# Kernel tuning notes

Measured on AMD Instinct MI355X. Metric: run time of the kernel, lower is better.

Reference implementation:

```python
import jax, jax.numpy as jnp
import numpy as np

N = 100000   # nodes
E = 1600000  # edges (avg degree 16)
D = 48       # in_channels
H = 256      # hidden_channels
HH = H // 2  # 128
OUT = 40     # out_channels


def _lin(key, fan_in, fan_out):
    return jax.random.normal(key, (fan_in, fan_out), jnp.float32) * (1.0 / np.sqrt(fan_in))


def setup_inputs() -> dict:
    key = jax.random.key(0)
    ks = jax.random.split(key, 8)
    node_feature = jax.random.normal(ks[0], (N, D), jnp.float32)
    edge_index = jax.random.randint(ks[1], (2, E), 0, N, dtype=jnp.int32)
    return {
        "node_feature": node_feature,
        "edge_index": edge_index,
        # mlp1: (D + D) -> H -> HH
        "W1a": _lin(ks[2], 2 * D, H), "b1a": jnp.zeros((H,), jnp.float32),
        "W1b": _lin(ks[3], H, HH),    "b1b": jnp.zeros((HH,), jnp.float32),
        # mlp2: (HH + HH + D) -> H -> HH
        "W2a": _lin(ks[4], 2 * HH + D, H), "b2a": jnp.zeros((H,), jnp.float32),
        "W2b": _lin(ks[5], H, HH),         "b2b": jnp.zeros((HH,), jnp.float32),
        # mlp3: (HH + HH + D) -> H -> OUT
        "W3a": _lin(ks[6], 2 * HH + D, H), "b3a": jnp.zeros((H,), jnp.float32),
        "W3b": _lin(ks[7], H, OUT),        "b3b": jnp.zeros((OUT,), jnp.float32),
    }


def _lgconv(x, src, dst):
    # LGConv(normalize=False): out[i] = sum_{(j,i) in E} x[j]
    return jax.ops.segment_sum(x[src], dst, num_segments=N)


def _mlp(x, Wa, ba, Wb, bb):
    # pyg MLP(-1, hidden, out): Linear -> ReLU -> Linear
    return jax.nn.relu(x @ Wa + ba) @ Wb + bb


def reference(node_feature, edge_index,
              W1a, b1a, W1b, b1b,
              W2a, b2a, W2b, b2b,
              W3a, b3a, W3b, b3b):
    src, dst = edge_index[0], edge_index[1]

    c1 = _lgconv(node_feature, src, dst)                    # [N, D]
    h1 = jax.nn.relu(_mlp(jnp.concatenate([c1, node_feature], axis=1),
                          W1a, b1a, W1b, b1b))              # [N, HH]

    c2 = _lgconv(h1, src, dst)                              # [N, HH]
    h2 = jax.nn.relu(_mlp(jnp.concatenate([c2, h1, node_feature], axis=1),
                          W2a, b2a, W2b, b2b))              # [N, HH]

    c3 = _lgconv(h2, src, dst)                              # [N, HH]
    logits = _mlp(jnp.concatenate([c3, h2, node_feature], axis=1),
                  W3a, b3a, W3b, b3b)                       # [N, OUT]
    return jax.nn.log_softmax(logits, axis=1)
```

## Files before the change

### kernel.cpp

```cpp
#include <hip/hip_runtime.h>
#include <math.h>

typedef __attribute__((ext_vector_type(8)))  short s16x8;
typedef __attribute__((ext_vector_type(16))) float f32x16;
typedef __attribute__((ext_vector_type(2)))  float f32x2;

__device__ inline unsigned short f2bf(float f) {
    unsigned u = __float_as_uint(f);
    u += 0x7fffu + ((u >> 16) & 1u);
    return (unsigned short)(u >> 16);
}
__device__ inline unsigned char f2fp8(float v) {
    return (unsigned char)(__builtin_amdgcn_cvt_pk_fp8_f32(v, v, 0, false) & 0xff);
}
__device__ inline void acc_fp8x8(float* a, uint2 v) {
    f32x2 p0 = __builtin_amdgcn_cvt_pk_f32_fp8(v.x, false);
    f32x2 p1 = __builtin_amdgcn_cvt_pk_f32_fp8(v.x, true);
    f32x2 p2 = __builtin_amdgcn_cvt_pk_f32_fp8(v.y, false);
    f32x2 p3 = __builtin_amdgcn_cvt_pk_f32_fp8(v.y, true);
    a[0] += p0.x; a[1] += p0.y; a[2] += p1.x; a[3] += p1.y;
    a[4] += p2.x; a[5] += p2.y; a[6] += p3.x; a[7] += p3.y;
}
__device__ inline uint4 fp8x8_to_bf16x8(uint2 v) {
    f32x2 p0 = __builtin_amdgcn_cvt_pk_f32_fp8(v.x, false);
    f32x2 p1 = __builtin_amdgcn_cvt_pk_f32_fp8(v.x, true);
    f32x2 p2 = __builtin_amdgcn_cvt_pk_f32_fp8(v.y, false);
    f32x2 p3 = __builtin_amdgcn_cvt_pk_f32_fp8(v.y, true);
    uint4 o;
    o.x = ((unsigned)f2bf(p0.y) << 16) | f2bf(p0.x);
    o.y = ((unsigned)f2bf(p1.y) << 16) | f2bf(p1.x);
    o.z = ((unsigned)f2bf(p2.y) << 16) | f2bf(p2.x);
    o.w = ((unsigned)f2bf(p3.y) << 16) | f2bf(p3.x);
    return o;
}

#define BMAX 3200
#define RNG  512

__global__ __launch_bounds__(256)
void prep_fused(const float* __restrict__ x,
                unsigned char* __restrict__ xq,
                const float* __restrict__ W1a, unsigned short* __restrict__ Wf1a,
                const float* __restrict__ W1b, unsigned short* __restrict__ Wf1b,
                const float* __restrict__ W2a, unsigned short* __restrict__ Wf2a,
                const float* __restrict__ W2b, unsigned short* __restrict__ Wf2b,
                const float* __restrict__ W3a, unsigned short* __restrict__ Wf3a,
                const float* __restrict__ W3b, unsigned short* __restrict__ Wf3b,
                int N) {
    int i = blockIdx.x * 256 + threadIdx.x;
    int nx = N * 48;
    if (i < nx) { xq[i] = f2fp8(x[i]); return; }
    i -= nx;
    if (i < 24576) {
        int j = i & 7, lane = (i >> 3) & 63, p = (i >> 9) & 1, sw = i >> 10;
        int s = sw % 6, w = sw / 6;
        int col = w * 64 + p * 32 + (lane & 31);
        int k   = s * 16 + (lane >> 5) * 8 + j;
        Wf1a[i] = f2bf(W1a[(size_t)k * 256 + col]); return;
    }
    i -= 24576;
    if (i < 32768) {
        int j = i & 7, lane = (i >> 3) & 63, sw = i >> 9;
        int s = sw & 15, w = sw >> 4;
        int col = w * 32 + (lane & 31);
        int k   = s * 16 + (lane >> 5) * 8 + j;
        Wf1b[i] = f2bf(W1b[(size_t)k * 128 + col]); return;
    }
    i -= 32768;
    if (i < 77824) {
        int j = i & 7, lane = (i >> 3) & 63, p = (i >> 9) & 1, sw = i >> 10;
        int s = sw % 19, w = sw / 19;
        int col = w * 64 + p * 32 + (lane & 31);
        int k   = s * 16 + (lane >> 5) * 8 + j;
        Wf2a[i] = f2bf(W2a[(size_t)k * 256 + col]); return;
    }
    i -= 77824;
    if (i < 32768) {
        int j = i & 7, lane = (i >> 3) & 63, sw = i >> 9;
        int s = sw & 15, w = sw >> 4;
        int col = w * 32 + (lane & 31);
        int k   = s * 16 + (lane >> 5) * 8 + j;
        Wf2b[i] = f2bf(W2b[(size_t)k * 128 + col]); return;
    }
    i -= 32768;
    if (i < 77824) {
        int j = i & 7, lane = (i >> 3) & 63, p = (i >> 9) & 1, sw = i >> 10;
        int s = sw % 19, w = sw / 19;
        int col = w * 64 + p * 32 + (lane & 31);
        int k   = s * 16 + (lane >> 5) * 8 + j;
        Wf3a[i] = f2bf(W3a[(size_t)k * 256 + col]); return;
    }
    i -= 77824;
    if (i < 16384) {
        int j = i & 7, lane = (i >> 3) & 63, sw = i >> 9;
        int s = sw & 15, w = sw >> 4;
        int col = w * 32 + (lane & 31);
        int k   = s * 16 + (lane >> 5) * 8 + j;
        float v = (col < 40) ? W3b[(size_t)k * 40 + col] : 0.f;
        Wf3b[i] = f2bf(v); return;
    }
}

__global__ __launch_bounds__(256)
void bucketize(const int* __restrict__ src, const int* __restrict__ dst,
               int2* __restrict__ pairs, int* __restrict__ offsg,
               int E, int C, int per) {
    __shared__ int sdst[BMAX];
    __shared__ int ssrc[BMAX];
    __shared__ int cnt[RNG];
    __shared__ int cur[RNG + 1];
    __shared__ int sh[256];
    const int p    = blockIdx.x;
    const int base = p * C;
    const int len  = min(C, E - base);
    const int t    = threadIdx.x;

    cnt[t] = 0; cnt[t + 256] = 0;
    for (int i = t; i < len; i += 256) { sdst[i] = dst[base + i]; ssrc[i] = src[base + i]; }
    __syncthreads();
    for (int i = t; i < len; i += 256) {
        int r = sdst[i] / per;
        atomicAdd(&cnt[r], 1);
    }
    __syncthreads();
    const int cA = cnt[2 * t], cB = cnt[2 * t + 1];
    sh[t] = cA + cB;
    __syncthreads();
    for (int off = 1; off < 256; off <<= 1) {
        int add = (t >= off) ? sh[t - off] : 0;
        __syncthreads();
        sh[t] += add;
        __syncthreads();
    }
    const int excl = sh[t] - cA - cB;
    cur[2 * t] = excl;
    cur[2 * t + 1] = excl + cA;
    if (t == 255) cur[RNG] = sh[255];
    offsg[p * (RNG + 1) + 2 * t]     = excl;
    offsg[p * (RNG + 1) + 2 * t + 1] = excl + cA;
    if (t == 255) offsg[p * (RNG + 1) + RNG] = sh[255];
    __syncthreads();
    for (int i = t; i < len; i += 256) {
        int d = sdst[i];
        int r = d / per;
        int pos = atomicAdd(&cur[r], 1);
        pairs[base + pos] = make_int2(ssrc[i], d);
    }
}

__global__ __launch_bounds__(256)
void range_tot(const int* __restrict__ offsg, int* __restrict__ rtot) {
    __shared__ int sh[256];
    const int r = blockIdx.x;
    const int t = threadIdx.x;
    int s = 0;
    for (int p = t; p < RNG; p += 256)
        s += offsg[p * (RNG + 1) + r + 1] - offsg[p * (RNG + 1) + r];
    sh[t] = s;
    __syncthreads();
    for (int off = 128; off >= 1; off >>= 1) {
        if (t < off) sh[t] += sh[t + off];
        __syncthreads();
    }
    if (t == 0) rtot[r] = sh[0];
}

__global__ __launch_bounds__(256)
void scan_rtot(int* __restrict__ rtot) {
    __shared__ int sh[256];
    const int t = threadIdx.x;
    const int a = rtot[2 * t], b = rtot[2 * t + 1];
    sh[t] = a + b;
    __syncthreads();
    for (int off = 1; off < 256; off <<= 1) {
        int add = (t >= off) ? sh[t - off] : 0;
        __syncthreads();
        sh[t] += add;
        __syncthreads();
    }
    const int excl = sh[t] - a - b;
    rtot[2 * t]     = excl;
    rtot[2 * t + 1] = excl + a;
}

__global__ __launch_bounds__(256)
void place_all(const int2* __restrict__ pairs, const int* __restrict__ offsg,
               const int* __restrict__ rbase,
               int* __restrict__ rowptr, int* __restrict__ deg,
               int* __restrict__ csr_src, int N, int C, int per, int E) {
    __shared__ int po[RNG];
    __shared__ int W[RNG + 1];
    __shared__ int sh[256];
    __shared__ int dcnt[256];
    __shared__ int curs[256];
    const int r  = blockIdx.x;
    const int lo = r * per;
    const int hi = min(lo + per, N);
    const int cnt = hi - lo;
    if (cnt <= 0) return;
    const int t = threadIdx.x;
    dcnt[t] = 0;
    const int pA = 2 * t, pB = 2 * t + 1;
    const int oA0 = offsg[pA * (RNG + 1) + r];
    const int oA1 = offsg[pA * (RNG + 1) + r + 1];
    const int oB0 = offsg[pB * (RNG + 1) + r];
    const int oB1 = offsg[pB * (RNG + 1) + r + 1];
    po[pA] = oA0; po[pB] = oB0;
    const int cA = oA1 - oA0, cB = oB1 - oB0;
    sh[t] = cA + cB;
    __syncthreads();
    for (int off = 1; off < 256; off <<= 1) {
        int add = (t >= off) ? sh[t - off] : 0;
        __syncthreads();
        sh[t] += add;
        __syncthreads();
    }
    const int excl = sh[t] - cA - cB;
    W[pA] = excl; W[pB] = excl + cA;
    if (t == 255) W[RNG] = sh[255];
    __syncthreads();
    const int tot = W[RNG];
    for (int i = t; i < tot; i += 256) {
        int a = 0, b = RNG;
        while (b - a > 1) { int m = (a + b) >> 1; if (W[m] <= i) a = m; else b = m; }
        const int2 pr = pairs[(size_t)a * C + po[a] + (i - W[a])];
        atomicAdd(&dcnt[pr.y - lo], 1);
    }
    __syncthreads();
    const int myc = dcnt[t];
    sh[t] = myc;
    __syncthreads();
    for (int off = 1; off < 256; off <<= 1) {
        int add = (t >= off) ? sh[t - off] : 0;
        __syncthreads();
        sh[t] += add;
        __syncthreads();
    }
    const int loc = sh[t] - myc;
    const int rb  = rbase[r];
    if (t < cnt) { rowptr[lo + t] = rb + loc; deg[lo + t] = myc; }
    curs[t] = rb + loc;
    __syncthreads();
    for (int i = t; i < tot; i += 256) {
        int a = 0, b = RNG;
        while (b - a > 1) { int m = (a + b) >> 1; if (W[m] <= i) a = m; else b = m; }
        const int2 pr = pairs[(size_t)a * C + po[a] + (i - W[a])];
        const int pos = atomicAdd(&curs[pr.y - lo], 1);
        if (pos < E) csr_src[pos] = pr.x;
    }
}

template<int D, int LPN>
__global__ __launch_bounds__(256)
void lgconv_gather_fp8(const unsigned char* __restrict__ xq,
                       const int* __restrict__ rowptr,
                       const int* __restrict__ deg,
                       const int* __restrict__ csr_src,
                       unsigned short* __restrict__ out, int N) {
    const int g    = (blockIdx.x * 256 + threadIdx.x) / LPN;
    const int lane = threadIdx.x & (LPN - 1);
    if (g >= N) return;
    if (lane * 8 >= D) return;
    const int start = rowptr[g];
    const int dg    = deg[g];
    const unsigned char* xb = xq + lane * 8;
    float acc[8] = {0.f,0.f,0.f,0.f,0.f,0.f,0.f,0.f};
    int j = 0;
    for (; j + 3 < dg; j += 4) {
        const int s0 = csr_src[start + j];
        const int s1 = csr_src[start + j + 1];
        const int s2 = csr_src[start + j + 2];
        const int s3 = csr_src[start + j + 3];
        uint2 v0 = *(const uint2*)(xb + (size_t)s0 * D);
        uint2 v1 = *(const uint2*)(xb + (size_t)s1 * D);
        uint2 v2 = *(const uint2*)(xb + (size_t)s2 * D);
        uint2 v3 = *(const uint2*)(xb + (size_t)s3 * D);
        acc_fp8x8(acc, v0); acc_fp8x8(acc, v1);
        acc_fp8x8(acc, v2); acc_fp8x8(acc, v3);
    }
    for (; j < dg; ++j) {
        const int s0 = csr_src[start + j];
        uint2 v0 = *(const uint2*)(xb + (size_t)s0 * D);
        acc_fp8x8(acc, v0);
    }
    uint4 o;
    o.x = ((unsigned)f2bf(acc[1]) << 16) | f2bf(acc[0]);
    o.y = ((unsigned)f2bf(acc[3]) << 16) | f2bf(acc[2]);
    o.z = ((unsigned)f2bf(acc[5]) << 16) | f2bf(acc[4]);
    o.w = ((unsigned)f2bf(acc[7]) << 16) | f2bf(acc[6]);
    *(uint4*)(out + (size_t)g * D + lane * 8) = o;
}

template<int LA, int LB, int LC, bool LSM>
__global__ __launch_bounds__(256)
void fused_mlp_mfma(const unsigned short* __restrict__ segA,
                    const unsigned char* __restrict__ segB,
                    const unsigned char* __restrict__ segC,
                    const unsigned short* __restrict__ WfA, const float* __restrict__ ba,
                    const unsigned short* __restrict__ WfB, const float* __restrict__ bb,
                    void* __restrict__ outv, unsigned char* __restrict__ outq,
                    int n) {
    constexpr int K1   = LA + LB + LC;
    constexpr int NS1  = K1 / 16;
    constexpr int NCH  = K1 / 8;
    constexpr int KPAD = K1 + 8;
    constexpr int K2P  = 264;
    constexpr int SW   = (32 * KPAD > 32 * K2P) ? 32 * KPAD : 32 * K2P;
    __shared__ __attribute__((aligned(16))) unsigned short smem[SW];
    unsigned short* Ab  = smem;
    unsigned short* hid = smem;

    const int tid  = threadIdx.x;
    const int wave = tid >> 6;
    const int lane = tid & 63;
    const int l31  = lane & 31;
    const int lh   = lane >> 5;
    const int row0 = blockIdx.x * 32;

    for (int c = tid; c < 32 * NCH; c += 256) {
        const int m  = c / NCH;
        const int kc = c - m * NCH;
        const int row = row0 + m;
        const int ra  = (row < n) ? row : (n - 1);
        uint4 val;
        if (kc * 8 < LA) {
            val = *(const uint4*)(segA + (size_t)ra * LA + kc * 8);
        } else {
            const unsigned char* qp;
            int koff;
            if (kc * 8 < LA + LB) { qp = segB + (size_t)ra * LB; koff = kc * 8 - LA; }
            else                  { qp = segC + (size_t)ra * LC; koff = kc * 8 - LA - LB; }
            val = fp8x8_to_bf16x8(*(const uint2*)(qp + koff));
        }
        *(uint4*)(Ab + m * KPAD + kc * 8) = val;
    }
    __syncthreads();

    f32x16 acc00 = {}, acc01 = {};
    const unsigned short* wfa = WfA + (size_t)wave * NS1 * 1024 + lane * 8;
    const int a0off = l31 * KPAD + lh * 8;

    #pragma unroll
    for (int s = 0; s < NS1; ++s) {
        s16x8 a0 = *(const s16x8*)(Ab + a0off + s * 16);
        s16x8 b0 = *(const s16x8*)(wfa + s * 1024);
        s16x8 b1 = *(const s16x8*)(wfa + s * 1024 + 512);
        acc00 = __builtin_amdgcn_mfma_f32_32x32x16_bf16(a0, b0, acc00, 0, 0, 0);
        acc01 = __builtin_amdgcn_mfma_f32_32x32x16_bf16(a0, b1, acc01, 0, 0, 0);
    }
    __syncthreads();

    {
        const int c0 = wave * 64 + l31;
        const int c1 = c0 + 32;
        const float bias0 = ba[c0];
        const float bias1 = ba[c1];
        #pragma unroll
        for (int t = 0; t < 16; ++t) {
            int rloc = (t & 3) + 8 * (t >> 2) + 4 * lh;
            hid[rloc * K2P + c0] = f2bf(fmaxf(acc00[t] + bias0, 0.f));
            hid[rloc * K2P + c1] = f2bf(fmaxf(acc01[t] + bias1, 0.f));
        }
    }
    __syncthreads();

    if (!LSM) {
        f32x16 d0 = {};
        const unsigned short* wfb = WfB + (size_t)wave * 16 * 512 + lane * 8;
        const int h0 = l31 * K2P + lh * 8;
        #pragma unroll
        for (int s = 0; s < 16; ++s) {
            s16x8 a0 = *(const s16x8*)&hid[h0 + s * 16];
            s16x8 b  = *(const s16x8*)(wfb + s * 512);
            d0 = __builtin_amdgcn_mfma_f32_32x32x16_bf16(a0, b, d0, 0, 0, 0);
        }
        const int col = wave * 32 + l31;
        const float bias = bb[col];
        #pragma unroll
        for (int t = 0; t < 16; ++t) {
            int rloc = (t & 3) + 8 * (t >> 2) + 4 * lh;
            int rr0 = row0 + rloc;
            if (rr0 < n)
                outq[(size_t)rr0 * 128 + col] = f2fp8(fmaxf(d0[t] + bias, 0.f));
        }
    } else {
        float* lg = (float*)smem;
        f32x16 d = {};
        if (wave < 2) {
            const unsigned short* wfb = WfB + (size_t)wave * 16 * 512 + lane * 8;
            const int h0 = l31 * K2P + lh * 8;
            #pragma unroll
            for (int s = 0; s < 16; ++s) {
                s16x8 a = *(const s16x8*)&hid[h0 + s * 16];
                s16x8 b = *(const s16x8*)(wfb + s * 512);
                d = __builtin_amdgcn_mfma_f32_32x32x16_bf16(a, b, d, 0, 0, 0);
            }
        }
        __syncthreads();
        if (wave < 2) {
            const int col = wave * 32 + l31;
            const float bias = (col < 40) ? bb[col] : 0.f;
            #pragma unroll
            for (int t = 0; t < 16; ++t) {
                int rloc = (t & 3) + 8 * (t >> 2) + 4 * lh;
                lg[rloc * 68 + col] = d[t] + bias;
            }
        }
        __syncthreads();
        const int r = tid >> 3, j = tid & 7;
        float mx = -1e30f;
        #pragma unroll
        for (int c = 0; c < 5; ++c) mx = fmaxf(mx, lg[r * 68 + j * 5 + c]);
        mx = fmaxf(mx, __shfl_xor(mx, 1));
        mx = fmaxf(mx, __shfl_xor(mx, 2));
        mx = fmaxf(mx, __shfl_xor(mx, 4));
        float sm = 0.f;
        #pragma unroll
        for (int c = 0; c < 5; ++c) sm += __expf(lg[r * 68 + j * 5 + c] - mx);
        sm += __shfl_xor(sm, 1);
        sm += __shfl_xor(sm, 2);
        sm += __shfl_xor(sm, 4);
        const float lse = mx + __logf(sm);
        const int row = row0 + r;
        float* out = (float*)outv;
        if (row < n) {
            #pragma unroll
            for (int c = 0; c < 5; ++c)
                out[(size_t)row * 40 + j * 5 + c] = lg[r * 68 + j * 5 + c] - lse;
        }
    }
}

extern "C" void kernel_launch(void* const* d_in, const int* in_sizes, int n_in,
                              void* d_out, int out_size, void* d_ws, size_t ws_size,
                              hipStream_t stream) {
    const float* x   = (const float*)d_in[0];
    const int*   ei  = (const int*)d_in[1];
    const float* W1a = (const float*)d_in[2];
    const float* b1a = (const float*)d_in[3];
    const float* W1b = (const float*)d_in[4];
    const float* b1b = (const float*)d_in[5];
    const float* W2a = (const float*)d_in[6];
    const float* b2a = (const float*)d_in[7];
    const float* W2b = (const float*)d_in[8];
    const float* b2b = (const float*)d_in[9];
    const float* W3a = (const float*)d_in[10];
    const float* b3a = (const float*)d_in[11];
    const float* W3b = (const float*)d_in[12];
    const float* b3b = (const float*)d_in[13];
    float* out = (float*)d_out;

    const int E = in_sizes[1] / 2;
    const int N = in_sizes[0] / 48;
    const int* src = ei;
    const int* dst = ei + E;

    const int nprod = RNG;
    const int C     = (E + nprod - 1) / nprod;
    const int per   = (N + RNG - 1) / RNG;

    char* p = (char*)d_ws;
    auto alloc = [&](size_t bytes) { void* q = p; p += (bytes + 255) & ~(size_t)255; return q; };
    unsigned char*  xq   = (unsigned char*) alloc((size_t)N * 48);
    unsigned short* c1   = (unsigned short*)alloc((size_t)N * 48  * 2);
    unsigned char*  h1q  = (unsigned char*) alloc((size_t)N * 128);
    unsigned short* c2   = (unsigned short*)alloc((size_t)N * 128 * 2);
    unsigned char*  h2q  = (unsigned char*) alloc((size_t)N * 128);
    unsigned short* Wf1a = (unsigned short*)alloc((size_t)24576 * 2);
    unsigned short* Wf1b = (unsigned short*)alloc((size_t)32768 * 2);
    unsigned short* Wf2a = (unsigned short*)alloc((size_t)77824 * 2);
    unsigned short* Wf2b = (unsigned short*)alloc((size_t)32768 * 2);
    unsigned short* Wf3a = (unsigned short*)alloc((size_t)77824 * 2);
    unsigned short* Wf3b = (unsigned short*)alloc((size_t)16384 * 2);
    int* deg     = (int*)alloc((size_t)N * 4);
    int* rowptr  = (int*)alloc((size_t)N * 4);
    int* rtot    = (int*)alloc((size_t)RNG * 4);
    int* csr_src = (int*)alloc((size_t)E * 4);
    int2* pairs  = (int2*)alloc((size_t)nprod * C * 8);
    int* offsg   = (int*)alloc((size_t)nprod * (RNG + 1) * 4);

    const int nblk32 = (N + 31) / 32;

    {
        int total = N * 48 + 24576 + 32768 + 77824 + 32768 + 77824 + 16384;
        prep_fused<<<(total + 255) / 256, 256, 0, stream>>>(
            x, xq, W1a, Wf1a, W1b, Wf1b, W2a, Wf2a, W2b, Wf2b,
            W3a, Wf3a, W3b, Wf3b, N);
    }

    bucketize<<<nprod, 256, 0, stream>>>(src, dst, pairs, offsg, E, C, per);
    range_tot<<<RNG, 256, 0, stream>>>(offsg, rtot);
    scan_rtot<<<1, 256, 0, stream>>>(rtot);
    place_all<<<RNG, 256, 0, stream>>>(pairs, offsg, rtot, rowptr, deg, csr_src,
                                       N, C, per, E);

    lgconv_gather_fp8<48, 8><<<((size_t)N * 8 + 255) / 256, 256, 0, stream>>>(
        xq, rowptr, deg, csr_src, c1, N);
    fused_mlp_mfma<48, 48, 0, false><<<nblk32, 256, 0, stream>>>(
        c1, xq, (const unsigned char*)nullptr, Wf1a, b1a, Wf1b, b1b,
        nullptr, h1q, N);

    lgconv_gather_fp8<128, 16><<<((size_t)N * 16 + 255) / 256, 256, 0, stream>>>(
        h1q, rowptr, deg, csr_src, c2, N);
    fused_mlp_mfma<128, 128, 48, false><<<nblk32, 256, 0, stream>>>(
        c2, h1q, xq, Wf2a, b2a, Wf2b, b2b, nullptr, h2q, N);

    lgconv_gather_fp8<128, 16><<<((size_t)N * 16 + 255) / 256, 256, 0, stream>>>(
        h2q, rowptr, deg, csr_src, c2, N);
    fused_mlp_mfma<128, 128, 48, true><<<nblk32, 256, 0, stream>>>(
        c2, h2q, xq, Wf3a, b3a, Wf3b, b3b, out, (unsigned char*)nullptr, N);
}
```

Before: 342.4 us.

## Fuse weight prep with bucketize, replace range_tot with atomics, unroll gather by 8

Edge bucketization now runs in the same launch as the feature and weight conversion. The first RNG blocks bucketize and the remaining blocks do the conversion. The separate range_tot reduction kernel is dropped: per-range totals are accumulated with global atomics into a zero-memset rtot. The fp8 gather loop is unrolled to 8 neighbours, with int4 vectorised index loads, to raise memory-level parallelism. The risks are unaligned int4 index loads at arbitrary row starts, and a hidden assumption that the bucketize block count equals RNG.

```diff
diff --git a/kernel.cpp b/kernel.cpp
--- a/kernel.cpp
+++ b/kernel.cpp
@@ -36,25 +36,76 @@
 
 #define BMAX 3200
 #define RNG  512
+#define WPREP 262144
 
 __global__ __launch_bounds__(256)
-void prep_fused(const float* __restrict__ x,
-                unsigned char* __restrict__ xq,
-                const float* __restrict__ W1a, unsigned short* __restrict__ Wf1a,
-                const float* __restrict__ W1b, unsigned short* __restrict__ Wf1b,
-                const float* __restrict__ W2a, unsigned short* __restrict__ Wf2a,
-                const float* __restrict__ W2b, unsigned short* __restrict__ Wf2b,
-                const float* __restrict__ W3a, unsigned short* __restrict__ Wf3a,
-                const float* __restrict__ W3b, unsigned short* __restrict__ Wf3b,
-                int N) {
-    int i = blockIdx.x * 256 + threadIdx.x;
+void prep_bucketize(const float* __restrict__ x, unsigned char* __restrict__ xq,
+                    const float* __restrict__ W1a, unsigned short* __restrict__ Wf1a,
+                    const float* __restrict__ W1b, unsigned short* __restrict__ Wf1b,
+                    const float* __restrict__ W2a, unsigned short* __restrict__ Wf2a,
+                    const float* __restrict__ W2b, unsigned short* __restrict__ Wf2b,
+                    const float* __restrict__ W3a, unsigned short* __restrict__ Wf3a,
+                    const float* __restrict__ W3b, unsigned short* __restrict__ Wf3b,
+                    const int* __restrict__ src, const int* __restrict__ dst,
+                    int2* __restrict__ pairs, int* __restrict__ offsg,
+                    int* __restrict__ rtot,
+                    int N, int E, int C, int per) {
+    __shared__ int sdst[BMAX];
+    __shared__ int ssrc[BMAX];
+    __shared__ int cnt[RNG];
+    __shared__ int cur[RNG + 1];
+    __shared__ int sh[256];
+    const int t = threadIdx.x;
+
+    if (blockIdx.x < RNG) {
+        const int p    = blockIdx.x;
+        const int base = p * C;
+        const int len  = min(C, E - base);
+
+        cnt[t] = 0; cnt[t + 256] = 0;
+        for (int i = t; i < len; i += 256) { sdst[i] = dst[base + i]; ssrc[i] = src[base + i]; }
+        __syncthreads();
+        for (int i = t; i < len; i += 256) {
+            int r = sdst[i] / per;
+            atomicAdd(&cnt[r], 1);
+        }
+        __syncthreads();
+        const int cA = cnt[2 * t], cB = cnt[2 * t + 1];
+        if (cA) atomicAdd(&rtot[2 * t], cA);
+        if (cB) atomicAdd(&rtot[2 * t + 1], cB);
+        sh[t] = cA + cB;
+        __syncthreads();
+        for (int off = 1; off < 256; off <<= 1) {
+            int add = (t >= off) ? sh[t - off] : 0;
+            __syncthreads();
+            sh[t] += add;
+            __syncthreads();
+        }
+        const int excl = sh[t] - cA - cB;
+        cur[2 * t] = excl;
+        cur[2 * t + 1] = excl + cA;
+        if (t == 255) cur[RNG] = sh[255];
+        offsg[p * (RNG + 1) + 2 * t]     = excl;
+        offsg[p * (RNG + 1) + 2 * t + 1] = excl + cA;
+        if (t == 255) offsg[p * (RNG + 1) + RNG] = sh[255];
+        __syncthreads();
+        for (int i = t; i < len; i += 256) {
+            int d = sdst[i];
+            int r = d / per;
+            int pos = atomicAdd(&cur[r], 1);
+            pairs[base + pos] = make_int2(ssrc[i], d);
+        }
+        return;
+    }
+
+    int i = (blockIdx.x - RNG) * 256 + t;
     int nx = N * 48;
     if (i < nx) { xq[i] = f2fp8(x[i]); return; }
     i -= nx;
     if (i < 24576) {
-        int j = i & 7, lane = (i >> 3) & 63, p = (i >> 9) & 1, sw = i >> 10;
+        int j = i & 7, lane = (i >> 3) & 63, pp = (i >> 9) & 1, sw = i >> 10;
         int s = sw % 6, w = sw / 6;
-        int col = w * 64 + p * 32 + (lane & 31);
+        int col = w * 64 + pp * 32 + (lane & 31);
         int k   = s * 16 + (lane >> 5) * 8 + j;
         Wf1a[i] = f2bf(W1a[(size_t)k * 256 + col]); return;
     }
@@ -68,9 +119,9 @@
     }
     i -= 32768;
     if (i < 77824) {
-        int j = i & 7, lane = (i >> 3) & 63, p = (i >> 9) & 1, sw = i >> 10;
+        int j = i & 7, lane = (i >> 3) & 63, pp = (i >> 9) & 1, sw = i >> 10;
         int s = sw % 19, w = sw / 19;
-        int col = w * 64 + p * 32 + (lane & 31);
+        int col = w * 64 + pp * 32 + (lane & 31);
         int k   = s * 16 + (lane >> 5) * 8 + j;
         Wf2a[i] = f2bf(W2a[(size_t)k * 256 + col]); return;
     }
@@ -84,9 +135,9 @@
     }
     i -= 32768;
     if (i < 77824) {
-        int j = i & 7, lane = (i >> 3) & 63, p = (i >> 9) & 1, sw = i >> 10;
+        int j = i & 7, lane = (i >> 3) & 63, pp = (i >> 9) & 1, sw = i >> 10;
         int s = sw % 19, w = sw / 19;
-        int col = w * 64 + p * 32 + (lane & 31);
+        int col = w * 64 + pp * 32 + (lane & 31);
         int k   = s * 16 + (lane >> 5) * 8 + j;
         Wf3a[i] = f2bf(W3a[(size_t)k * 256 + col]); return;
     }
@@ -99,70 +150,6 @@
         float v = (col < 40) ? W3b[(size_t)k * 40 + col] : 0.f;
         Wf3b[i] = f2bf(v); return;
     }
-}
-
-__global__ __launch_bounds__(256)
-void bucketize(const int* __restrict__ src, const int* __restrict__ dst,
-               int2* __restrict__ pairs, int* __restrict__ offsg,
-               int E, int C, int per) {
-    __shared__ int sdst[BMAX];
-    __shared__ int ssrc[BMAX];
-    __shared__ int cnt[RNG];
-    __shared__ int cur[RNG + 1];
-    __shared__ int sh[256];
-    const int p    = blockIdx.x;
-    const int base = p * C;
-    const int len  = min(C, E - base);
-    const int t    = threadIdx.x;
-
-    cnt[t] = 0; cnt[t + 256] = 0;
-    for (int i = t; i < len; i += 256) { sdst[i] = dst[base + i]; ssrc[i] = src[base + i]; }
-    __syncthreads();
-    for (int i = t; i < len; i += 256) {
-        int r = sdst[i] / per;
-        atomicAdd(&cnt[r], 1);
-    }
-    __syncthreads();
-    const int cA = cnt[2 * t], cB = cnt[2 * t + 1];
-    sh[t] = cA + cB;
-    __syncthreads();
-    for (int off = 1; off < 256; off <<= 1) {
-        int add = (t >= off) ? sh[t - off] : 0;
-        __syncthreads();
-        sh[t] += add;
-        __syncthreads();
-    }
-    const int excl = sh[t] - cA - cB;
-    cur[2 * t] = excl;
-    cur[2 * t + 1] = excl + cA;
-    if (t == 255) cur[RNG] = sh[255];
-    offsg[p * (RNG + 1) + 2 * t]     = excl;
-    offsg[p * (RNG + 1) + 2 * t + 1] = excl + cA;
-    if (t == 255) offsg[p * (RNG + 1) + RNG] = sh[255];
-    __syncthreads();
-    for (int i = t; i < len; i += 256) {
-        int d = sdst[i];
-        int r = d / per;
-        int pos = atomicAdd(&cur[r], 1);
-        pairs[base + pos] = make_int2(ssrc[i], d);
-    }
-}
-
-__global__ __launch_bounds__(256)
-void range_tot(const int* __restrict__ offsg, int* __restrict__ rtot) {
-    __shared__ int sh[256];
-    const int r = blockIdx.x;
-    const int t = threadIdx.x;
-    int s = 0;
-    for (int p = t; p < RNG; p += 256)
-        s += offsg[p * (RNG + 1) + r + 1] - offsg[p * (RNG + 1) + r];
-    sh[t] = s;
-    __syncthreads();
-    for (int off = 128; off >= 1; off >>= 1) {
-        if (t < off) sh[t] += sh[t + off];
-        __syncthreads();
-    }
-    if (t == 0) rtot[r] = sh[0];
 }
 
 __global__ __launch_bounds__(256)
@@ -266,17 +253,31 @@
     const unsigned char* xb = xq + lane * 8;
     float acc[8] = {0.f,0.f,0.f,0.f,0.f,0.f,0.f,0.f};
     int j = 0;
-    for (; j + 3 < dg; j += 4) {
-        const int s0 = csr_src[start + j];
-        const int s1 = csr_src[start + j + 1];
-        const int s2 = csr_src[start + j + 2];
-        const int s3 = csr_src[start + j + 3];
-        uint2 v0 = *(const uint2*)(xb + (size_t)s0 * D);
-        uint2 v1 = *(const uint2*)(xb + (size_t)s1 * D);
-        uint2 v2 = *(const uint2*)(xb + (size_t)s2 * D);
-        uint2 v3 = *(const uint2*)(xb + (size_t)s3 * D);
+    for (; j + 7 < dg; j += 8) {
+        const int4 ia = *(const int4*)(csr_src + start + j);
+        const int4 ib = *(const int4*)(csr_src + start + j + 4);
+        uint2 v0 = *(const uint2*)(xb + (size_t)ia.x * D);
+        uint2 v1 = *(const uint2*)(xb + (size_t)ia.y * D);
+        uint2 v2 = *(const uint2*)(xb + (size_t)ia.z * D);
+        uint2 v3 = *(const uint2*)(xb + (size_t)ia.w * D);
+        uint2 v4 = *(const uint2*)(xb + (size_t)ib.x * D);
+        uint2 v5 = *(const uint2*)(xb + (size_t)ib.y * D);
+        uint2 v6 = *(const uint2*)(xb + (size_t)ib.z * D);
+        uint2 v7 = *(const uint2*)(xb + (size_t)ib.w * D);
         acc_fp8x8(acc, v0); acc_fp8x8(acc, v1);
         acc_fp8x8(acc, v2); acc_fp8x8(acc, v3);
+        acc_fp8x8(acc, v4); acc_fp8x8(acc, v5);
+        acc_fp8x8(acc, v6); acc_fp8x8(acc, v7);
+    }
+    if (j + 3 < dg) {
+        const int4 ia = *(const int4*)(csr_src + start + j);
+        uint2 v0 = *(const uint2*)(xb + (size_t)ia.x * D);
+        uint2 v1 = *(const uint2*)(xb + (size_t)ia.y * D);
+        uint2 v2 = *(const uint2*)(xb + (size_t)ia.z * D);
+        uint2 v3 = *(const uint2*)(xb + (size_t)ia.w * D);
+        acc_fp8x8(acc, v0); acc_fp8x8(acc, v1);
+        acc_fp8x8(acc, v2); acc_fp8x8(acc, v3);
+        j += 4;
     }
     for (; j < dg; ++j) {
         const int s0 = csr_src[start + j];
@@ -481,15 +482,14 @@
 
     const int nblk32 = (N + 31) / 32;
 
+    hipMemsetAsync(rtot, 0, RNG * sizeof(int), stream);
     {
-        int total = N * 48 + 24576 + 32768 + 77824 + 32768 + 77824 + 16384;
-        prep_fused<<<(total + 255) / 256, 256, 0, stream>>>(
+        int prep_total = N * 48 + WPREP;
+        int nblk = RNG + (prep_total + 255) / 256;
+        prep_bucketize<<<nblk, 256, 0, stream>>>(
             x, xq, W1a, Wf1a, W1b, Wf1b, W2a, Wf2a, W2b, Wf2b,
-            W3a, Wf3a, W3b, Wf3b, N);
-    }
-
-    bucketize<<<nprod, 256, 0, stream>>>(src, dst, pairs, offsg, E, C, per);
-    range_tot<<<RNG, 256, 0, stream>>>(offsg, rtot);
+            W3a, Wf3a, W3b, Wf3b, src, dst, pairs, offsg, rtot, N, E, C, per);
+    }
     scan_rtot<<<1, 256, 0, stream>>>(rtot);
     place_all<<<RNG, 256, 0, stream>>>(pairs, offsg, rtot, rowptr, deg, csr_src,
                                        N, C, per, E);
```

Result: no change. 346.7 us (+1.2%).
